# Kernel tuning notes

Hardware: AMD Instinct MI355X
Metric: run time of the kernel (lower is better)

The kernel has to match this reference:

```python
import jax, jax.numpy as jnp
import numpy as np
import math

N_HEAD = 16
N_FEAT = 1024
O_FEAT = 1024
D_K = N_FEAT // N_HEAD


def setup_inputs() -> dict:
    key = jax.random.key(0)
    ks = jax.random.split(key, 11)
    B, L, DIN = 4, 2048, 1024
    s_in = 1.0 / math.sqrt(DIN)
    s_f = 1.0 / math.sqrt(N_FEAT)
    return {
        "query": jax.random.normal(ks[0], (B, L, DIN), jnp.float32),
        "key": jax.random.normal(ks[1], (B, L, DIN), jnp.float32),
        "value": jax.random.normal(ks[2], (B, L, DIN), jnp.float32),
        "Wq": jax.random.uniform(ks[3], (DIN, N_FEAT), jnp.float32, -s_in, s_in),
        "bq": jax.random.uniform(ks[4], (N_FEAT,), jnp.float32, -s_in, s_in),
        "Wk": jax.random.uniform(ks[5], (DIN, N_FEAT), jnp.float32, -s_in, s_in),
        "bk": jax.random.uniform(ks[6], (N_FEAT,), jnp.float32, -s_in, s_in),
        "Wv": jax.random.uniform(ks[7], (DIN, N_FEAT), jnp.float32, -s_in, s_in),
        "bv": jax.random.uniform(ks[8], (N_FEAT,), jnp.float32, -s_in, s_in),
        "Wo": jax.random.uniform(ks[9], (N_FEAT, O_FEAT), jnp.float32, -s_f, s_f),
        "bo": jax.random.uniform(ks[10], (O_FEAT,), jnp.float32, -s_f, s_f),
    }


def reference(query, key, value, Wq, bq, Wk, bk, Wv, bv, Wo, bo):
    B = query.shape[0]
    # QKV projections -> [B, H, L, Dk]
    def proj(x, W, b):
        y = x @ W + b
        return y.reshape(B, -1, N_HEAD, D_K).transpose(0, 2, 1, 3)
    q = proj(query, Wq, bq)
    k = proj(key, Wk, bk)
    v = proj(value, Wv, bv)
    # naive attention: full [B,H,Lq,Lk] scores
    scores = jnp.einsum("bhqd,bhkd->bhqk", q, k) / math.sqrt(D_K)
    attn = jax.nn.softmax(scores, axis=-1)  # dropout_rate=0 -> identity
    x = jnp.einsum("bhqk,bhkd->bhqd", attn, v)
    x = x.transpose(0, 2, 1, 3).reshape(B, -1, N_FEAT)
    return x @ Wo + bo
```

## Files before the change

### kernel.cpp

```cpp
#include <hip/hip_runtime.h>
#include <hip/hip_bf16.h>

#define DM 1024
#define LQ 2048

typedef __attribute__((ext_vector_type(8))) short short8;
typedef __attribute__((ext_vector_type(4))) float floatx4;

#define MFMA16(a, b, c) __builtin_amdgcn_mfma_f32_16x16x32_bf16((a), (b), (c), 0, 0, 0)

__device__ __forceinline__ unsigned short f2b(float f) {
  union { float f; unsigned u; } x; x.f = f;
  unsigned u = x.u;
  unsigned r = (u + 0x7fffu + ((u >> 16) & 1u)) >> 16;
  return (unsigned short)r;
}
__device__ __forceinline__ float b2f(unsigned short h) {
  union { unsigned u; float f; } x; x.u = ((unsigned)h) << 16;
  return x.f;
}

__device__ __forceinline__ unsigned pk2(float f0, float f1) {
  union { float f; unsigned u; } a, b; a.f = f0; b.f = f1;
  return __builtin_amdgcn_perm(b.u + 0x8000u, a.u + 0x8000u, 0x07060302u);
}
__device__ __forceinline__ uint4 pack16(float4 a, float4 b) {
  return make_uint4(pk2(a.x, a.y), pk2(a.z, a.w), pk2(b.x, b.y), pk2(b.z, b.w));
}

__device__ __forceinline__ void gl_lds16(const void* g, void* l) {
  __builtin_amdgcn_global_load_lds(
      (const __attribute__((address_space(1))) void*)g,
      (__attribute__((address_space(3))) void*)l, 16, 0, 0);
}

__global__ __launch_bounds__(256) void transpose_w4(
    const float* __restrict__ W0, const float* __restrict__ W1,
    const float* __restrict__ W2, const float* __restrict__ W3,
    unsigned short* __restrict__ T0, unsigned short* __restrict__ T1,
    unsigned short* __restrict__ T2, unsigned short* __restrict__ T3) {
  __shared__ unsigned short t[64][65];
  const float* src; unsigned short* dst;
  switch (blockIdx.z) {
    case 0: src = W0; dst = T0; break;
    case 1: src = W1; dst = T1; break;
    case 2: src = W2; dst = T2; break;
    default: src = W3; dst = T3; break;
  }
  const int x = threadIdx.x & 63;
  const int y4 = threadIdx.x >> 6;
  const int c0 = blockIdx.x * 64;
  const int r0 = blockIdx.y * 64;
#pragma unroll
  for (int i = 0; i < 16; ++i) {
    int r = y4 * 16 + i;
    t[r][x] = f2b(src[(size_t)(r0 + r) * 1024 + c0 + x]);
  }
  __syncthreads();
#pragma unroll
  for (int i = 0; i < 16; ++i) {
    int r = y4 * 16 + i;
    dst[(size_t)(c0 + r) * 1024 + r0 + x] = t[x][r];
  }
}

__global__ __launch_bounds__(256) void gemm_qkv(
    const float* __restrict__ Aq, const float* __restrict__ Ak,
    const float* __restrict__ Av,
    const unsigned short* __restrict__ BtQ, const unsigned short* __restrict__ BtK,
    const unsigned short* __restrict__ BtV,
    const float* __restrict__ bq, const float* __restrict__ bk,
    const float* __restrict__ bv,
    unsigned short* __restrict__ Qb, unsigned short* __restrict__ Kb,
    unsigned short* __restrict__ Vt) {
  const int K = 1024, N = 1024;
  __shared__ unsigned short As[128 * 32];
  __shared__ unsigned short Bs[128 * 32];
  const int z = blockIdx.z;
  const float* A; const unsigned short* Bt; const float* bias;
  if (z == 0) { A = Aq; Bt = BtQ; bias = bq; }
  else if (z == 1) { A = Ak; Bt = BtK; bias = bk; }
  else { A = Av; Bt = BtV; bias = bv; }

  const int tid = threadIdx.x;
  const int wave = tid >> 6;
  const int lane = tid & 63;
  const int fm = lane & 15;
  const int quad = lane >> 4;
  const int m0 = blockIdx.y * 128;
  const int n0 = blockIdx.x * 128;
  const int wm = (wave >> 1) * 64;
  const int wn = (wave & 1) * 64;

  floatx4 acc[4][4];
#pragma unroll
  for (int i = 0; i < 4; ++i)
#pragma unroll
    for (int j = 0; j < 4; ++j) acc[i][j] = (floatx4){0.f, 0.f, 0.f, 0.f};

  const int srow = lane >> 2;
  const int scol = (lane & 3) * 8;
  const float* Ag = A + (size_t)(m0 + wave * 32 + srow) * K + scol;
  const unsigned short* Bg = Bt + (size_t)(n0 + wave * 32 + srow) * K + scol;
  unsigned short* AsB = &As[(wave * 32) * 32];
  unsigned short* Bsl = &Bs[(wave * 32) * 32];

  for (int k0 = 0; k0 < K; k0 += 32) {
    float4 f0 = *(const float4*)(Ag + k0);
    float4 f1 = *(const float4*)(Ag + k0 + 4);
    float4 f2 = *(const float4*)(Ag + k0 + (size_t)16 * K);
    float4 f3 = *(const float4*)(Ag + k0 + (size_t)16 * K + 4);
    gl_lds16(Bg + k0, Bsl);
    gl_lds16(Bg + k0 + (size_t)16 * K, Bsl + 16 * 32);
    *(uint4*)&AsB[lane * 8] = pack16(f0, f1);
    *(uint4*)&AsB[16 * 32 + lane * 8] = pack16(f2, f3);
    __syncthreads();
    short8 a[4], b[4];
#pragma unroll
    for (int i = 0; i < 4; ++i)
      a[i] = *(const short8*)&As[(wm + i * 16 + fm) * 32 + quad * 8];
#pragma unroll
    for (int j = 0; j < 4; ++j)
      b[j] = *(const short8*)&Bs[(wn + j * 16 + fm) * 32 + quad * 8];
#pragma unroll
    for (int i = 0; i < 4; ++i)
#pragma unroll
      for (int j = 0; j < 4; ++j) acc[i][j] = MFMA16(a[i], b[j], acc[i][j]);
    __syncthreads();
  }

  float bvv[4];
#pragma unroll
  for (int j = 0; j < 4; ++j) bvv[j] = bias[n0 + wn + j * 16 + fm];

  if (z < 2) {
    unsigned short* C = (z == 0) ? Qb : Kb;
#pragma unroll
    for (int i = 0; i < 4; ++i) {
      int row = m0 + wm + i * 16 + quad * 4;
#pragma unroll
      for (int j = 0; j < 4; ++j) {
        int col = n0 + wn + j * 16 + fm;
#pragma unroll
        for (int r = 0; r < 4; ++r)
          C[(size_t)(row + r) * N + col] = f2b(acc[i][j][r] + bvv[j]);
      }
    }
  } else {
#pragma unroll
    for (int i = 0; i < 4; ++i) {
      int row = m0 + wm + i * 16 + quad * 4;
      int b = row >> 11, l = row & 2047;
#pragma unroll
      for (int j = 0; j < 4; ++j) {
        int col = n0 + wn + j * 16 + fm;
        int h = col >> 6, d = col & 63;
        uint2 pk;
        pk.x = pk2(acc[i][j][0] + bvv[j], acc[i][j][1] + bvv[j]);
        pk.y = pk2(acc[i][j][2] + bvv[j], acc[i][j][3] + bvv[j]);
        *(uint2*)&Vt[(((size_t)b * 16 + h) * 64 + d) * 2048 + l] = pk;
      }
    }
  }
}

__global__ __launch_bounds__(256) void gemm_bt_bias_f32(
    const unsigned short* __restrict__ A, const unsigned short* __restrict__ Bt,
    const float* __restrict__ bias, float* __restrict__ C,
    int M, int N, int K) {
  __shared__ unsigned short As[128 * 32];
  __shared__ unsigned short Bs[128 * 32];
  const int tid = threadIdx.x;
  const int wave = tid >> 6;
  const int lane = tid & 63;
  const int fm = lane & 15;
  const int quad = lane >> 4;
  const int m0 = blockIdx.y * 128;
  const int n0 = blockIdx.x * 128;
  const int wm = (wave >> 1) * 64;
  const int wn = (wave & 1) * 64;

  floatx4 acc[4][4];
#pragma unroll
  for (int i = 0; i < 4; ++i)
#pragma unroll
    for (int j = 0; j < 4; ++j) acc[i][j] = (floatx4){0.f, 0.f, 0.f, 0.f};

  const int srow = lane >> 2;
  const int scol = (lane & 3) * 8;
  const unsigned short* Ag = A + (size_t)(m0 + wave * 32 + srow) * K + scol;
  const unsigned short* Bg = Bt + (size_t)(n0 + wave * 32 + srow) * K + scol;
  unsigned short* Asl = &As[(wave * 32) * 32];
  unsigned short* Bsl = &Bs[(wave * 32) * 32];

  for (int k0 = 0; k0 < K; k0 += 32) {
    gl_lds16(Ag + k0, Asl);
    gl_lds16(Ag + k0 + (size_t)16 * K, Asl + 16 * 32);
    gl_lds16(Bg + k0, Bsl);
    gl_lds16(Bg + k0 + (size_t)16 * K, Bsl + 16 * 32);
    __syncthreads();
    short8 a[4], b[4];
#pragma unroll
    for (int i = 0; i < 4; ++i)
      a[i] = *(const short8*)&As[(wm + i * 16 + fm) * 32 + quad * 8];
#pragma unroll
    for (int j = 0; j < 4; ++j)
      b[j] = *(const short8*)&Bs[(wn + j * 16 + fm) * 32 + quad * 8];
#pragma unroll
    for (int i = 0; i < 4; ++i)
#pragma unroll
      for (int j = 0; j < 4; ++j) acc[i][j] = MFMA16(a[i], b[j], acc[i][j]);
    __syncthreads();
  }

  float bv[4];
#pragma unroll
  for (int j = 0; j < 4; ++j) bv[j] = bias[n0 + wn + j * 16 + fm];
#pragma unroll
  for (int i = 0; i < 4; ++i) {
    int row = m0 + wm + i * 16 + quad * 4;
#pragma unroll
    for (int j = 0; j < 4; ++j) {
      int col = n0 + wn + j * 16 + fm;
#pragma unroll
      for (int r = 0; r < 4; ++r)
        C[(size_t)(row + r) * N + col] = acc[i][j][r] + bv[j];
    }
  }
}

__global__ __launch_bounds__(256, 4) void attn_kernel(
    const unsigned short* Qb, const unsigned short* __restrict__ Kb,
    const unsigned short* __restrict__ Vtg, unsigned short* Xb) {
  __shared__ unsigned short Ks[64 * 72];
  __shared__ unsigned short Vts[64 * 72];
  __shared__ unsigned short Ps[4 * 32 * 72];
  unsigned short* Qs = Ps;

  const int tid = threadIdx.x;
  const int wave = tid >> 6;
  const int lane = tid & 63;
  const int fm = lane & 15;
  const int quad = lane >> 4;
  const int qt = blockIdx.x;
  const int bh = blockIdx.y;
  const size_t base = (size_t)(bh >> 4) * (LQ * DM) + (size_t)(bh & 15) * 64;
  const unsigned short* Vg = Vtg + (size_t)bh * 64 * 2048;
  const int q0 = qt * 128;

#pragma unroll
  for (int it = 0; it < 4; ++it) {
    int idx = it * 256 + tid;
    int r = idx >> 3;
    int cc = (idx & 7) * 8;
    *(short8*)&Qs[r * 72 + cc] =
        *(const short8*)(Qb + base + (size_t)(q0 + r) * DM + cc);
  }
  __syncthreads();
  short8 qf[2][2];
#pragma unroll
  for (int mt = 0; mt < 2; ++mt)
#pragma unroll
    for (int ks = 0; ks < 2; ++ks)
      qf[mt][ks] = *(const short8*)&Qs[(wave * 32 + mt * 16 + fm) * 72 + ks * 32 + quad * 8];
  __syncthreads();

  float llocal[2] = {0.f, 0.f};
  floatx4 oacc[4][2];
#pragma unroll
  for (int dt = 0; dt < 4; ++dt)
#pragma unroll
    for (int mt = 0; mt < 2; ++mt) oacc[dt][mt] = (floatx4){0.f, 0.f, 0.f, 0.f};

  const float csc = 0.1803368801111204f;
  unsigned short* Pw = &Ps[wave * 32 * 72];

  const int srow0 = tid >> 3;
  const int scc = (tid & 7) * 8;
  short8 kr[2], vr[2];
#pragma unroll
  for (int it = 0; it < 2; ++it) {
    int row = it * 32 + srow0;
    kr[it] = *(const short8*)(Kb + base + (size_t)row * DM + scc);
    vr[it] = *(const short8*)(Vg + (size_t)row * 2048 + scc);
  }

  for (int kt = 0; kt < 32; ++kt) {
    __syncthreads();
#pragma unroll
    for (int it = 0; it < 2; ++it) {
      int row = it * 32 + srow0;
      *(short8*)&Ks[row * 72 + scc] = kr[it];
      *(short8*)&Vts[row * 72 + scc] = vr[it];
    }
    __syncthreads();
    if (kt < 31) {
      int k0n = (kt + 1) * 64;
#pragma unroll
      for (int it = 0; it < 2; ++it) {
        int row = it * 32 + srow0;
        kr[it] = *(const short8*)(Kb + base + (size_t)(k0n + row) * DM + scc);
        vr[it] = *(const short8*)(Vg + (size_t)row * 2048 + k0n + scc);
      }
    }

    floatx4 sacc[4][2];
#pragma unroll
    for (int jt = 0; jt < 4; ++jt)
#pragma unroll
      for (int mt = 0; mt < 2; ++mt) sacc[jt][mt] = (floatx4){0.f, 0.f, 0.f, 0.f};
#pragma unroll
    for (int jt = 0; jt < 4; ++jt) {
      short8 k0f = *(const short8*)&Ks[(jt * 16 + fm) * 72 + quad * 8];
      short8 k1f = *(const short8*)&Ks[(jt * 16 + fm) * 72 + 32 + quad * 8];
#pragma unroll
      for (int mt = 0; mt < 2; ++mt) {
        sacc[jt][mt] = MFMA16(k0f, qf[mt][0], sacc[jt][mt]);
        sacc[jt][mt] = MFMA16(k1f, qf[mt][1], sacc[jt][mt]);
      }
    }

#pragma unroll
    for (int mt = 0; mt < 2; ++mt) {
      int rowoff = (mt * 16 + fm) * 72;
      float ll = 0.f;
#pragma unroll
      for (int jt = 0; jt < 4; ++jt) {
        float p0 = exp2f(sacc[jt][mt][0] * csc);
        float p1 = exp2f(sacc[jt][mt][1] * csc);
        float p2 = exp2f(sacc[jt][mt][2] * csc);
        float p3 = exp2f(sacc[jt][mt][3] * csc);
        uint2 pk;
        pk.x = pk2(p0, p1);
        pk.y = pk2(p2, p3);
        *(uint2*)&Pw[rowoff + jt * 16 + quad * 4] = pk;
        ll += (p0 + p1) + (p2 + p3);
      }
      llocal[mt] += ll;
    }

    __threadfence_block();

#pragma unroll
    for (int ks = 0; ks < 2; ++ks) {
      short8 pf0 = *(const short8*)&Pw[fm * 72 + ks * 32 + quad * 8];
      short8 pf1 = *(const short8*)&Pw[(16 + fm) * 72 + ks * 32 + quad * 8];
#pragma unroll
      for (int dt = 0; dt < 4; ++dt) {
        short8 vf = *(const short8*)&Vts[(dt * 16 + fm) * 72 + ks * 32 + quad * 8];
        oacc[dt][0] = MFMA16(vf, pf0, oacc[dt][0]);
        oacc[dt][1] = MFMA16(vf, pf1, oacc[dt][1]);
      }
    }
  }

  float inv[2];
#pragma unroll
  for (int mt = 0; mt < 2; ++mt) {
    float l = llocal[mt];
    l += __shfl_xor(l, 16);
    l += __shfl_xor(l, 32);
    inv[mt] = 1.0f / l;
  }

#pragma unroll
  for (int mt = 0; mt < 2; ++mt) {
    int q = q0 + wave * 32 + mt * 16 + fm;
#pragma unroll
    for (int dt = 0; dt < 4; ++dt) {
      uint2 o;
      o.x = pk2(oacc[dt][mt][0] * inv[mt], oacc[dt][mt][1] * inv[mt]);
      o.y = pk2(oacc[dt][mt][2] * inv[mt], oacc[dt][mt][3] * inv[mt]);
      *(uint2*)&Xb[base + (size_t)q * DM + dt * 16 + quad * 4] = o;
    }
  }
}

extern "C" void kernel_launch(void* const* d_in, const int* in_sizes, int n_in,
                              void* d_out, int out_size, void* d_ws, size_t ws_size,
                              hipStream_t stream) {
  const float* q_in = (const float*)d_in[0];
  const float* k_in = (const float*)d_in[1];
  const float* v_in = (const float*)d_in[2];
  const float* Wq = (const float*)d_in[3];
  const float* bq = (const float*)d_in[4];
  const float* Wk = (const float*)d_in[5];
  const float* bk = (const float*)d_in[6];
  const float* Wv = (const float*)d_in[7];
  const float* bv = (const float*)d_in[8];
  const float* Wo = (const float*)d_in[9];
  const float* bo = (const float*)d_in[10];
  float* out = (float*)d_out;

  char* w = (char*)d_ws;
  unsigned short* WqT = (unsigned short*)w; w += 1024 * 1024 * 2;
  unsigned short* WkT = (unsigned short*)w; w += 1024 * 1024 * 2;
  unsigned short* WvT = (unsigned short*)w; w += 1024 * 1024 * 2;
  unsigned short* WoT = (unsigned short*)w; w += 1024 * 1024 * 2;
  unsigned short* Qb  = (unsigned short*)w; w += (size_t)8192 * 1024 * 2;
  unsigned short* Kb  = (unsigned short*)w; w += (size_t)8192 * 1024 * 2;
  unsigned short* Vt  = (unsigned short*)w; w += (size_t)8192 * 1024 * 2;
  unsigned short* Xb  = Qb;

  transpose_w4<<<dim3(16, 16, 4), 256, 0, stream>>>(Wq, Wk, Wv, Wo,
                                                    WqT, WkT, WvT, WoT);

  gemm_qkv<<<dim3(8, 64, 3), 256, 0, stream>>>(
      q_in, k_in, v_in, WqT, WkT, WvT, bq, bk, bv, Qb, Kb, Vt);

  attn_kernel<<<dim3(16, 64), 256, 0, stream>>>(Qb, Kb, Vt, Xb);

  gemm_bt_bias_f32<<<dim3(8, 64), 256, 0, stream>>>(Xb, WoT, bo, out, 8192, 1024, 1024);
}
```

Before: 418.4 us.

## Fold softmax scale into Q projection, compute row sums via MFMA

Folds the 1/sqrt(dk)*log2(e) scale into the Q projection epilogue so the attention loop calls the raw hardware exp2 with no multiply. Replaces the per-element scalar row-sum accumulation and the final cross-lane shuffles with an extra MFMA against a vector of bf16 ones, adding two MFMAs per k-step. Swaps the manual perm-based bf16 packing for the native v_cvt_pk_bf16_f32 instruction. The goal is to cut VALU work in the softmax inner loop, at the cost of row sums now being taken over bf16-rounded probabilities and Q being rounded after scaling.

```diff
diff --git a/kernel.cpp b/kernel.cpp
--- a/kernel.cpp
+++ b/kernel.cpp
@@ -15,17 +15,15 @@
   unsigned r = (u + 0x7fffu + ((u >> 16) & 1u)) >> 16;
   return (unsigned short)r;
 }
-__device__ __forceinline__ float b2f(unsigned short h) {
-  union { unsigned u; float f; } x; x.u = ((unsigned)h) << 16;
-  return x.f;
-}
-
-__device__ __forceinline__ unsigned pk2(float f0, float f1) {
-  union { float f; unsigned u; } a, b; a.f = f0; b.f = f1;
-  return __builtin_amdgcn_perm(b.u + 0x8000u, a.u + 0x8000u, 0x07060302u);
+
+__device__ __forceinline__ unsigned cvt_pk(float lo, float hi) {
+  unsigned r;
+  asm("v_cvt_pk_bf16_f32 %0, %1, %2" : "=v"(r) : "v"(lo), "v"(hi));
+  return r;
 }
 __device__ __forceinline__ uint4 pack16(float4 a, float4 b) {
-  return make_uint4(pk2(a.x, a.y), pk2(a.z, a.w), pk2(b.x, b.y), pk2(b.z, b.w));
+  return make_uint4(cvt_pk(a.x, a.y), cvt_pk(a.z, a.w),
+                    cvt_pk(b.x, b.y), cvt_pk(b.z, b.w));
 }
 
 __device__ __forceinline__ void gl_lds16(const void* g, void* l) {
@@ -134,6 +132,7 @@
   for (int j = 0; j < 4; ++j) bvv[j] = bias[n0 + wn + j * 16 + fm];
 
   if (z < 2) {
+    const float sc = (z == 0) ? 0.1803368801111204f : 1.0f;
     unsigned short* C = (z == 0) ? Qb : Kb;
 #pragma unroll
     for (int i = 0; i < 4; ++i) {
@@ -143,7 +142,7 @@
         int col = n0 + wn + j * 16 + fm;
 #pragma unroll
         for (int r = 0; r < 4; ++r)
-          C[(size_t)(row + r) * N + col] = f2b(acc[i][j][r] + bvv[j]);
+          C[(size_t)(row + r) * N + col] = f2b((acc[i][j][r] + bvv[j]) * sc);
       }
     }
   } else {
@@ -156,8 +155,8 @@
         int col = n0 + wn + j * 16 + fm;
         int h = col >> 6, d = col & 63;
         uint2 pk;
-        pk.x = pk2(acc[i][j][0] + bvv[j], acc[i][j][1] + bvv[j]);
-        pk.y = pk2(acc[i][j][2] + bvv[j], acc[i][j][3] + bvv[j]);
+        pk.x = cvt_pk(acc[i][j][0] + bvv[j], acc[i][j][1] + bvv[j]);
+        pk.y = cvt_pk(acc[i][j][2] + bvv[j], acc[i][j][3] + bvv[j]);
         *(uint2*)&Vt[(((size_t)b * 16 + h) * 64 + d) * 2048 + l] = pk;
       }
     }
@@ -265,14 +264,19 @@
       qf[mt][ks] = *(const short8*)&Qs[(wave * 32 + mt * 16 + fm) * 72 + ks * 32 + quad * 8];
   __syncthreads();
 
-  float llocal[2] = {0.f, 0.f};
+  short8 ones;
+#pragma unroll
+  for (int i = 0; i < 8; ++i) ones[i] = (short)0x3F80;
+
+  floatx4 lacc[2];
+  lacc[0] = (floatx4){0.f, 0.f, 0.f, 0.f};
+  lacc[1] = (floatx4){0.f, 0.f, 0.f, 0.f};
   floatx4 oacc[4][2];
 #pragma unroll
   for (int dt = 0; dt < 4; ++dt)
 #pragma unroll
     for (int mt = 0; mt < 2; ++mt) oacc[dt][mt] = (floatx4){0.f, 0.f, 0.f, 0.f};
 
-  const float csc = 0.1803368801111204f;
   unsigned short* Pw = &Ps[wave * 32 * 72];
 
   const int srow0 = tid >> 3;
@@ -323,20 +327,17 @@
 #pragma unroll
     for (int mt = 0; mt < 2; ++mt) {
       int rowoff = (mt * 16 + fm) * 72;
-      float ll = 0.f;
 #pragma unroll
       for (int jt = 0; jt < 4; ++jt) {
-        float p0 = exp2f(sacc[jt][mt][0] * csc);
-        float p1 = exp2f(sacc[jt][mt][1] * csc);
-        float p2 = exp2f(sacc[jt][mt][2] * csc);
-        float p3 = exp2f(sacc[jt][mt][3] * csc);
+        float p0 = __builtin_amdgcn_exp2f(sacc[jt][mt][0]);
+        float p1 = __builtin_amdgcn_exp2f(sacc[jt][mt][1]);
+        float p2 = __builtin_amdgcn_exp2f(sacc[jt][mt][2]);
+        float p3 = __builtin_amdgcn_exp2f(sacc[jt][mt][3]);
         uint2 pk;
-        pk.x = pk2(p0, p1);
-        pk.y = pk2(p2, p3);
+        pk.x = cvt_pk(p0, p1);
+        pk.y = cvt_pk(p2, p3);
         *(uint2*)&Pw[rowoff + jt * 16 + quad * 4] = pk;
-        ll += (p0 + p1) + (p2 + p3);
-      }
-      llocal[mt] += ll;
+      }
     }
 
     __threadfence_block();
@@ -345,6 +346,8 @@
     for (int ks = 0; ks < 2; ++ks) {
       short8 pf0 = *(const short8*)&Pw[fm * 72 + ks * 32 + quad * 8];
       short8 pf1 = *(const short8*)&Pw[(16 + fm) * 72 + ks * 32 + quad * 8];
+      lacc[0] = MFMA16(ones, pf0, lacc[0]);
+      lacc[1] = MFMA16(ones, pf1, lacc[1]);
 #pragma unroll
       for (int dt = 0; dt < 4; ++dt) {
         short8 vf = *(const short8*)&Vts[(dt * 16 + fm) * 72 + ks * 32 + quad * 8];
@@ -355,13 +358,8 @@
   }
 
   float inv[2];
-#pragma unroll
-  for (int mt = 0; mt < 2; ++mt) {
-    float l = llocal[mt];
-    l += __shfl_xor(l, 16);
-    l += __shfl_xor(l, 32);
-    inv[mt] = 1.0f / l;
-  }
+  inv[0] = 1.0f / lacc[0][0];
+  inv[1] = 1.0f / lacc[1][0];
 
 #pragma unroll
   for (int mt = 0; mt < 2; ++mt) {
@@ -369,8 +367,8 @@
 #pragma unroll
     for (int dt = 0; dt < 4; ++dt) {
       uint2 o;
-      o.x = pk2(oacc[dt][mt][0] * inv[mt], oacc[dt][mt][1] * inv[mt]);
-      o.y = pk2(oacc[dt][mt][2] * inv[mt], oacc[dt][mt][3] * inv[mt]);
+      o.x = cvt_pk(oacc[dt][mt][0] * inv[mt], oacc[dt][mt][1] * inv[mt]);
+      o.y = cvt_pk(oacc[dt][mt][2] * inv[mt], oacc[dt][mt][3] * inv[mt]);
       *(uint2*)&Xb[base + (size_t)q * DM + dt * 16 + quad * 4] = o;
     }
   }
```

After: 378.4 us. 9.5% less time.
